# Kernel optimization log

Measured on AMD Instinct MI355X. Metric: run time of the kernel, lower is better.

## Reference

```python
import jax, jax.numpy as jnp
import numpy as np

N_NODES = 100000


def gcn_conv(x, edge_index, W, b, n_nodes):
    # GCNConv: out = D^{-1/2} (A + I) D^{-1/2} X W + b  (add_self_loops=True)
    xw = x @ W  # [N, F_out]
    loop = jnp.arange(n_nodes, dtype=edge_index.dtype)
    row = jnp.concatenate([edge_index[0], loop])  # source
    col = jnp.concatenate([edge_index[1], loop])  # target
    ones = jnp.ones(row.shape[0], dtype=x.dtype)
    deg = jax.ops.segment_sum(ones, col, num_segments=n_nodes)
    dinv = jnp.where(deg > 0, jax.lax.rsqrt(deg), 0.0)
    norm = dinv[row] * dinv[col]  # [E+N]
    msgs = norm[:, None] * xw[row]  # gather + scale
    out = jax.ops.segment_sum(msgs, col, num_segments=n_nodes)  # scatter-add
    return out + b


def setup_inputs() -> dict:
    key = jax.random.key(0)
    k1, k2, k3, k4 = jax.random.split(key, 4)
    x = jax.random.normal(k1, (N_NODES, 512), dtype=jnp.float32)
    edge_index = jax.random.randint(k2, (2, 3200000), 0, N_NODES, dtype=jnp.int64)
    W1 = jax.random.normal(k3, (512, 16), dtype=jnp.float32) * (1.0 / np.sqrt(512))
    b1 = jnp.zeros((16,), dtype=jnp.float32)
    W2 = jax.random.normal(k4, (16, 7), dtype=jnp.float32) * (1.0 / np.sqrt(16))
    b2 = jnp.zeros((7,), dtype=jnp.float32)
    return {"x": x, "edge_index": edge_index, "W1": W1, "b1": b1, "W2": W2, "b2": b2}


def reference(x, edge_index, W1, b1, W2, b2):
    n = x.shape[0]
    h = gcn_conv(x, edge_index, W1, b1, n)
    h = jax.nn.relu(h)
    # F.dropout(training=self.training) is identity in eval mode
    h = gcn_conv(h, edge_index, W2, b2, n)
    return jax.nn.log_softmax(h, axis=1)
```

## Files before the change

kernel.cpp:

```cpp
#include <hip/hip_runtime.h>
#include <math.h>
#include <stdint.h>

#define NBMAX 512
#define BCAP 10240

typedef __attribute__((ext_vector_type(8))) short short8;
typedef __attribute__((ext_vector_type(4))) float f32x4;

__device__ __forceinline__ unsigned int f2bf(float f) {
    unsigned int u = __float_as_uint(f);
    return (u + 0x7FFFu + ((u >> 16) & 1u)) >> 16;
}
__device__ __forceinline__ float bl(unsigned int u) { return __uint_as_float(u << 16); }
__device__ __forceinline__ float bh(unsigned int u) { return __uint_as_float(u & 0xFFFF0000u); }

__global__ void k_zero(int* __restrict__ p, int n) {
    int i = threadIdx.x;
    if (i < n) p[i] = 0;
}

__global__ __launch_bounds__(256) void k_hist_gemm(
    const int* __restrict__ col, int* __restrict__ bucketCnt, int E, int hB, int NB,
    const float* __restrict__ x, const float* __restrict__ W1,
    float* __restrict__ xw, int n) {
    __shared__ union {
        int hist[NBMAX];
        struct { uint4 bhi[1024]; uint4 blo[1024]; } g;
    } sh;
    if (blockIdx.x < hB) {
        for (int t = threadIdx.x; t < NB; t += 256) sh.hist[t] = 0;
        __syncthreads();
        int base = blockIdx.x * 4096;
#pragma unroll
        for (int i = 0; i < 16; ++i) {
            int e = base + threadIdx.x + i * 256;
            if (e < E) atomicAdd(&sh.hist[col[e] >> 8], 1);
        }
        __syncthreads();
        for (int t = threadIdx.x; t < NB; t += 256) {
            int c = sh.hist[t];
            if (c) atomicAdd(&bucketCnt[t], c);
        }
        return;
    }
    for (int s = threadIdx.x; s < 1024; s += 256) {
        int ts = s >> 6, l = s & 63;
        int colc = l & 15, kg = l >> 4;
        int kbase = ts * 32 + kg * 8;
        unsigned int hw[8], lw[8];
#pragma unroll
        for (int j = 0; j < 8; ++j) {
            float wv = W1[(size_t)(kbase + j) * 16 + colc];
            unsigned int u = __float_as_uint(wv);
            unsigned int h = u >> 16;
            unsigned int lo = f2bf(wv - bl(h));
            hw[j] = h; lw[j] = lo;
        }
        uint4 ph, pl;
        ph.x = hw[0] | (hw[1] << 16); ph.y = hw[2] | (hw[3] << 16);
        ph.z = hw[4] | (hw[5] << 16); ph.w = hw[6] | (hw[7] << 16);
        pl.x = lw[0] | (lw[1] << 16); pl.y = lw[2] | (lw[3] << 16);
        pl.z = lw[4] | (lw[5] << 16); pl.w = lw[6] | (lw[7] << 16);
        sh.g.bhi[s] = ph; sh.g.blo[s] = pl;
    }
    __syncthreads();

    int w = threadIdx.x >> 6, lane = threadIdx.x & 63;
    int mtMax = (n + 15) >> 4;
    int mt = (blockIdx.x - hB) * 4 + w;
    if (mt >= mtMax) return;
    int rowbase = mt * 16;
    int r0 = rowbase + (lane & 15);
    if (r0 >= n) r0 = n - 1;
    int kg = lane >> 4;
    const float4* xr = (const float4*)(x + (size_t)r0 * 512);
    f32x4 acc = {0.f, 0.f, 0.f, 0.f};
#pragma unroll 2
    for (int ts = 0; ts < 16; ++ts) {
        float4 u = xr[ts * 8 + kg * 2];
        float4 v = xr[ts * 8 + kg * 2 + 1];
        float e[8] = {u.x, u.y, u.z, u.w, v.x, v.y, v.z, v.w};
        short8 ah, al;
#pragma unroll
        for (int j = 0; j < 8; ++j) {
            unsigned int uu = __float_as_uint(e[j]);
            unsigned int h = uu >> 16;
            unsigned int lo = f2bf(e[j] - bl(h));
            ah[j] = (short)h;
            al[j] = (short)lo;
        }
        uint4 bhw = sh.g.bhi[ts * 64 + lane];
        uint4 blw = sh.g.blo[ts * 64 + lane];
        short8 bhv = *reinterpret_cast<const short8*>(&bhw);
        short8 blv = *reinterpret_cast<const short8*>(&blw);
        acc = __builtin_amdgcn_mfma_f32_16x16x32_bf16(ah, bhv, acc, 0, 0, 0);
        acc = __builtin_amdgcn_mfma_f32_16x16x32_bf16(al, bhv, acc, 0, 0, 0);
        acc = __builtin_amdgcn_mfma_f32_16x16x32_bf16(ah, blv, acc, 0, 0, 0);
    }
#pragma unroll
    for (int r = 0; r < 4; ++r) {
        int orow = rowbase + kg * 4 + r;
        if (orow < n) xw[(size_t)orow * 16 + (lane & 15)] = acc[r];
    }
}

__global__ void k_scanB(const int* __restrict__ bucketCnt, int* __restrict__ baseB,
                        int* __restrict__ cursor, int* __restrict__ offs,
                        int NB, int N, int E) {
    __shared__ int s[512];
    int t = threadIdx.x;
    int c = (t < NB) ? bucketCnt[t] : 0;
    s[t] = c;
    __syncthreads();
    for (int o = 1; o < 512; o <<= 1) {
        int v = (t >= o) ? s[t - o] : 0;
        __syncthreads();
        s[t] += v;
        __syncthreads();
    }
    if (t < NB) { int ex = s[t] - c; baseB[t] = ex; cursor[t] = ex; }
    if (t == NB) baseB[NB] = E;
    if (t == 0) offs[N] = E;
}

__global__ __launch_bounds__(512) void k_bucket(
    const int* __restrict__ row, const int* __restrict__ col,
    int* __restrict__ cursor, unsigned int* __restrict__ sortedG, int E, int NB) {
    __shared__ int histL[NBMAX];
    __shared__ int offsL[NBMAX];
    __shared__ int gbL[NBMAX];
    __shared__ int sbuf[512];
    __shared__ unsigned int stageW[4096];
    __shared__ unsigned short stageB[4096];
    int t = threadIdx.x;
    for (int i = t; i < NB; i += 512) histL[i] = 0;
    __syncthreads();
    int off = blockIdx.x * 4096;
    unsigned int w[8]; int bk[8]; int rk[8];
#pragma unroll
    for (int i = 0; i < 8; ++i) {
        int e = off + t + i * 512;
        if (e < E) {
            int c = col[e], r = row[e];
            w[i]  = ((unsigned int)r << 8) | (unsigned int)(c & 255);
            bk[i] = c >> 8;
            rk[i] = atomicAdd(&histL[bk[i]], 1);
        } else bk[i] = -1;
    }
    __syncthreads();
    int cnt = (t < NB) ? histL[t] : 0;
    sbuf[t] = cnt;
    __syncthreads();
    for (int o = 1; o < 512; o <<= 1) {
        int v = (t >= o) ? sbuf[t - o] : 0;
        __syncthreads();
        sbuf[t] += v;
        __syncthreads();
    }
    if (t < NB) {
        offsL[t] = sbuf[t] - cnt;
        gbL[t]   = cnt ? atomicAdd(&cursor[t], cnt) : 0;
    }
    __syncthreads();
#pragma unroll
    for (int i = 0; i < 8; ++i) {
        if (bk[i] >= 0) {
            int s2 = offsL[bk[i]] + rk[i];
            stageW[s2] = w[i];
            stageB[s2] = (unsigned short)bk[i];
        }
    }
    __syncthreads();
    int total = min(4096, E - off);
    for (int s2 = t; s2 < total; s2 += 512) {
        int b = stageB[s2];
        sortedG[gbL[b] + (s2 - offsL[b])] = stageW[s2];
    }
}

__global__ __launch_bounds__(512) void k_sortscale(
    unsigned int* __restrict__ sortedG, const int* __restrict__ baseB,
    int* __restrict__ offs, float* __restrict__ dinv,
    const float* __restrict__ xw, unsigned int* __restrict__ sxwh, int N) {
    __shared__ unsigned int wv[BCAP];
    __shared__ int hist[256];
    __shared__ int off_[256];
    __shared__ int sc[256];
    __shared__ float ds[256];
    int t = threadIdx.x, b = blockIdx.x;
    if (t < 256) hist[t] = 0;
    __syncthreads();
    int beg = baseB[b], end = baseB[b + 1];
    int cnt = end - beg;
    for (int i = t; i < cnt; i += 512) {
        unsigned int w = sortedG[beg + i];
        wv[i] = w;
        atomicAdd(&hist[w & 255], 1);
    }
    __syncthreads();
    if (t < 256) sc[t] = hist[t];
    __syncthreads();
    for (int o = 1; o < 256; o <<= 1) {
        int v = 0;
        if (t < 256 && t >= o) v = sc[t - o];
        __syncthreads();
        if (t < 256) sc[t] += v;
        __syncthreads();
    }
    if (t < 256) {
        off_[t] = sc[t] - hist[t];
        int node = b * 256 + t;
        float dv = rsqrtf((float)(hist[t] + 1));
        ds[t] = dv;
        if (node < N) { offs[node] = beg + off_[t]; dinv[node] = dv; }
        hist[t] = 0;
    }
    __syncthreads();
    for (int i = t; i < cnt; i += 512) {
        unsigned int w = wv[i];
        int c = w & 255;
        int r2 = atomicAdd(&hist[c], 1);
        sortedG[beg + off_[c] + r2] = w >> 8;
    }
    const float4* xw4 = (const float4*)xw;
    uint2* dsth = (uint2*)sxwh;
#pragma unroll
    for (int k = 0; k < 2; ++k) {
        int idx = t + k * 512;
        int nl  = idx >> 2;
        int node = b * 256 + nl;
        if (node < N) {
            float s = ds[nl];
            float4 v = xw4[(size_t)b * 1024 + idx];
            unsigned int u0 = f2bf(v.x * s), u1 = f2bf(v.y * s);
            unsigned int u2 = f2bf(v.z * s), u3 = f2bf(v.w * s);
            uint2 o; o.x = u0 | (u1 << 16); o.y = u2 | (u3 << 16);
            dsth[(size_t)b * 1024 + idx] = o;
        }
    }
}

__global__ __launch_bounds__(256) void k_gather1f(
    const int* __restrict__ offs, const int* __restrict__ srow,
    const uint4* __restrict__ s4, const float* __restrict__ dinv,
    const float* __restrict__ W2, const float* __restrict__ b1,
    float* __restrict__ sxw2p, int N) {
    __shared__ float sW2[112];
    __shared__ float sb1[16];
    if (threadIdx.x < 112) sW2[threadIdx.x] = W2[threadIdx.x];
    if (threadIdx.x < 16) sb1[threadIdx.x] = b1[threadIdx.x];
    __syncthreads();
    int idx = blockIdx.x * 256 + threadIdx.x;
    int node = idx >> 2, sub = idx & 3;
    int q = sub & 1, seg = sub >> 1;
    if (node >= N) return;
    int beg0 = offs[node], end0 = offs[node + 1];
    int mid = beg0 + ((end0 - beg0) >> 1);
    int beg = seg ? mid : beg0;
    int end = seg ? end0 : mid;

    float a0 = 0.f, a1 = 0.f, a2 = 0.f, a3 = 0.f;
    float a4 = 0.f, a5 = 0.f, a6 = 0.f, a7 = 0.f;
    if (seg == 0) {
        uint4 sv = s4[(size_t)node * 2 + q];
        a0 = bl(sv.x); a1 = bh(sv.x); a2 = bl(sv.y); a3 = bh(sv.y);
        a4 = bl(sv.z); a5 = bh(sv.z); a6 = bl(sv.w); a7 = bh(sv.w);
    }
    int j = beg;
    for (; j + 3 < end; j += 4) {
        int r0 = srow[j], r1 = srow[j + 1], r2 = srow[j + 2], r3 = srow[j + 3];
        uint4 v0 = s4[(size_t)r0 * 2 + q];
        uint4 v1 = s4[(size_t)r1 * 2 + q];
        uint4 v2 = s4[(size_t)r2 * 2 + q];
        uint4 v3 = s4[(size_t)r3 * 2 + q];
        a0 += (bl(v0.x) + bl(v1.x)) + (bl(v2.x) + bl(v3.x));
        a1 += (bh(v0.x) + bh(v1.x)) + (bh(v2.x) + bh(v3.x));
        a2 += (bl(v0.y) + bl(v1.y)) + (bl(v2.y) + bl(v3.y));
        a3 += (bh(v0.y) + bh(v1.y)) + (bh(v2.y) + bh(v3.y));
        a4 += (bl(v0.z) + bl(v1.z)) + (bl(v2.z) + bl(v3.z));
        a5 += (bh(v0.z) + bh(v1.z)) + (bh(v2.z) + bh(v3.z));
        a6 += (bl(v0.w) + bl(v1.w)) + (bl(v2.w) + bl(v3.w));
        a7 += (bh(v0.w) + bh(v1.w)) + (bh(v2.w) + bh(v3.w));
    }
    for (; j < end; ++j) {
        int r = srow[j];
        uint4 v = s4[(size_t)r * 2 + q];
        a0 += bl(v.x); a1 += bh(v.x); a2 += bl(v.y); a3 += bh(v.y);
        a4 += bl(v.z); a5 += bh(v.z); a6 += bl(v.w); a7 += bh(v.w);
    }
    a0 += __shfl_xor(a0, 2, 64); a1 += __shfl_xor(a1, 2, 64);
    a2 += __shfl_xor(a2, 2, 64); a3 += __shfl_xor(a3, 2, 64);
    a4 += __shfl_xor(a4, 2, 64); a5 += __shfl_xor(a5, 2, 64);
    a6 += __shfl_xor(a6, 2, 64); a7 += __shfl_xor(a7, 2, 64);
    float d = dinv[node];
    float h[8];
    h[0] = fmaxf(fmaf(d, a0, sb1[q * 8 + 0]), 0.f);
    h[1] = fmaxf(fmaf(d, a1, sb1[q * 8 + 1]), 0.f);
    h[2] = fmaxf(fmaf(d, a2, sb1[q * 8 + 2]), 0.f);
    h[3] = fmaxf(fmaf(d, a3, sb1[q * 8 + 3]), 0.f);
    h[4] = fmaxf(fmaf(d, a4, sb1[q * 8 + 4]), 0.f);
    h[5] = fmaxf(fmaf(d, a5, sb1[q * 8 + 5]), 0.f);
    h[6] = fmaxf(fmaf(d, a6, sb1[q * 8 + 6]), 0.f);
    h[7] = fmaxf(fmaf(d, a7, sb1[q * 8 + 7]), 0.f);
    float o[7] = {0.f, 0.f, 0.f, 0.f, 0.f, 0.f, 0.f};
    int rbase = q * 8;
#pragma unroll
    for (int i = 0; i < 8; ++i) {
        float hv = h[i];
#pragma unroll
        for (int jj = 0; jj < 7; ++jj) o[jj] = fmaf(hv, sW2[(rbase + i) * 7 + jj], o[jj]);
    }
#pragma unroll
    for (int jj = 0; jj < 7; ++jj) o[jj] += __shfl_xor(o[jj], 1, 64);
    if (seg == 0) {
        float4 wv4;
        if (q == 0) { wv4.x = o[0] * d; wv4.y = o[1] * d; wv4.z = o[2] * d; wv4.w = o[3] * d; }
        else        { wv4.x = o[4] * d; wv4.y = o[5] * d; wv4.z = o[6] * d; wv4.w = 0.f; }
        ((float4*)sxw2p)[(size_t)node * 2 + q] = wv4;
    }
}

__global__ __launch_bounds__(256) void k_gather2f(
    const int* __restrict__ offs, const int* __restrict__ srow,
    const float* __restrict__ sxw2p, const float* __restrict__ dinv,
    const float* __restrict__ b2, float* __restrict__ out, int N) {
    __shared__ float sb2[8];
    if (threadIdx.x < 7) sb2[threadIdx.x] = b2[threadIdx.x];
    if (threadIdx.x == 7) sb2[7] = 0.f;
    __syncthreads();
    int idx = blockIdx.x * 256 + threadIdx.x;
    int node = idx >> 2, sub = idx & 3;
    int q = sub & 1, seg = sub >> 1;
    if (node >= N) return;
    int beg0 = offs[node], end0 = offs[node + 1];
    int mid = beg0 + ((end0 - beg0) >> 1);
    int beg = seg ? mid : beg0;
    int end = seg ? end0 : mid;
    const float4* s4 = (const float4*)sxw2p;
    float4 a = {0.f, 0.f, 0.f, 0.f};
    if (seg == 0) a = s4[(size_t)node * 2 + q];
    int j = beg;
    for (; j + 3 < end; j += 4) {
        int r0 = srow[j], r1 = srow[j + 1], r2 = srow[j + 2], r3 = srow[j + 3];
        float4 v0 = s4[(size_t)r0 * 2 + q];
        float4 v1 = s4[(size_t)r1 * 2 + q];
        float4 v2 = s4[(size_t)r2 * 2 + q];
        float4 v3 = s4[(size_t)r3 * 2 + q];
        a.x += (v0.x + v1.x) + (v2.x + v3.x);
        a.y += (v0.y + v1.y) + (v2.y + v3.y);
        a.z += (v0.z + v1.z) + (v2.z + v3.z);
        a.w += (v0.w + v1.w) + (v2.w + v3.w);
    }
    for (; j < end; ++j) {
        int r = srow[j];
        float4 v = s4[(size_t)r * 2 + q];
        a.x += v.x; a.y += v.y; a.z += v.z; a.w += v.w;
    }
    a.x += __shfl_xor(a.x, 2, 64); a.y += __shfl_xor(a.y, 2, 64);
    a.z += __shfl_xor(a.z, 2, 64); a.w += __shfl_xor(a.w, 2, 64);
    float d = dinv[node];
    float z0 = fmaf(d, a.x, sb2[q * 4 + 0]);
    float z1 = fmaf(d, a.y, sb2[q * 4 + 1]);
    float z2 = fmaf(d, a.z, sb2[q * 4 + 2]);
    float z3 = (q == 0) ? fmaf(d, a.w, sb2[3]) : -INFINITY;
    float m = fmaxf(fmaxf(z0, z1), fmaxf(z2, z3));
    m = fmaxf(m, __shfl_xor(m, 1, 64));
    float s = expf(z0 - m) + expf(z1 - m) + expf(z2 - m) + ((q == 0) ? expf(z3 - m) : 0.f);
    s += __shfl_xor(s, 1, 64);
    float l = m + logf(s);
    if (seg == 0) {
        float* ob = out + (size_t)node * 7;
        if (q == 0) { ob[0] = z0 - l; ob[1] = z1 - l; ob[2] = z2 - l; ob[3] = z3 - l; }
        else        { ob[4] = z0 - l; ob[5] = z1 - l; ob[6] = z2 - l; }
    }
}

extern "C" void kernel_launch(void* const* d_in, const int* in_sizes, int n_in,
                              void* d_out, int out_size, void* d_ws, size_t ws_size,
                              hipStream_t stream) {
    const float* x  = (const float*)d_in[0];
    const int*   ei = (const int*)d_in[1];
    const float* W1 = (const float*)d_in[2];
    const float* b1 = (const float*)d_in[3];
    const float* W2 = (const float*)d_in[4];
    const float* b2 = (const float*)d_in[5];

    int N = in_sizes[0] / 512;
    int E = in_sizes[1] / 2;
    const int* row = ei;
    const int* col = ei + E;

    int NB = (N + 255) >> 8;

    int* bucketCnt = (int*)d_ws;
    int* baseB     = bucketCnt + 512;
    int* cursor    = baseB + 512;
    int* offs      = cursor + 512;
    unsigned int* sortedG = (unsigned int*)(offs + ((N + 4) & ~3));
    float* dinv  = (float*)(sortedG + E);
    float* xw1   = dinv + N;
    unsigned int* sxwh = (unsigned int*)(xw1 + (size_t)16 * N);
    float* sxw2p = xw1;
    float* out   = (float*)d_out;

    int hB = (E + 4095) / 4096;
    int mtMax = (N + 15) / 16;
    int gM = (mtMax + 3) / 4;
    int bB = (E + 4095) / 4096;
    int gP = (4 * N + 255) / 256;

    k_zero     <<<1, 512, 0, stream>>>(bucketCnt, NB);
    k_hist_gemm<<<hB + gM, 256, 0, stream>>>(col, bucketCnt, E, hB, NB, x, W1, xw1, N);
    k_scanB    <<<1, 512, 0, stream>>>(bucketCnt, baseB, cursor, offs, NB, N, E);
    k_bucket   <<<bB, 512, 0, stream>>>(row, col, cursor, sortedG, E, NB);
    k_sortscale<<<NB, 512, 0, stream>>>(sortedG, baseB, offs, dinv, xw1, sxwh, N);
    k_gather1f <<<gP, 256, 0, stream>>>(offs, (const int*)sortedG, (const uint4*)sxwh,
                                        dinv, W2, b1, sxw2p, N);
    k_gather2f <<<gP, 256, 0, stream>>>(offs, (const int*)sortedG, sxw2p, dinv, b2, out, N);
}
```

Measured before the change: 435.6 us.

## Split histogram from GEMM and stage x tiles through swizzled LDS

Separates the fused histogram+GEMM launch into two kernels, so the GEMM blocks no longer share a launch with histogram blocks. The GEMM now loads 64-row tiles of x coalesced (32 threads per row chunk) and converts them once to bf16 hi/lo. It stores them in an XOR-swizzled LDS layout, and the MFMA fragments read from there instead of each lane doing strided float4 loads per row. This aims to improve global-load coalescing on the 200MB x read, at the cost of an extra launch, more LDS use and extra barriers.

```diff
diff --git a/kernel.cpp b/kernel.cpp
--- a/kernel.cpp
+++ b/kernel.cpp
@@ -20,34 +20,37 @@
     if (i < n) p[i] = 0;
 }
 
-__global__ __launch_bounds__(256) void k_hist_gemm(
-    const int* __restrict__ col, int* __restrict__ bucketCnt, int E, int hB, int NB,
+__global__ __launch_bounds__(256) void k_hist(
+    const int* __restrict__ col, int* __restrict__ bucketCnt, int E, int NB) {
+    __shared__ int histL[NBMAX];
+    for (int t = threadIdx.x; t < NB; t += 256) histL[t] = 0;
+    __syncthreads();
+    int base = blockIdx.x * 4096;
+#pragma unroll
+    for (int i = 0; i < 16; ++i) {
+        int e = base + threadIdx.x + i * 256;
+        if (e < E) atomicAdd(&histL[col[e] >> 8], 1);
+    }
+    __syncthreads();
+    for (int t = threadIdx.x; t < NB; t += 256) {
+        int c = histL[t];
+        if (c) atomicAdd(&bucketCnt[t], c);
+    }
+}
+
+__global__ __launch_bounds__(256) void k_gemm(
     const float* __restrict__ x, const float* __restrict__ W1,
     float* __restrict__ xw, int n) {
-    __shared__ union {
-        int hist[NBMAX];
-        struct { uint4 bhi[1024]; uint4 blo[1024]; } g;
-    } sh;
-    if (blockIdx.x < hB) {
-        for (int t = threadIdx.x; t < NB; t += 256) sh.hist[t] = 0;
-        __syncthreads();
-        int base = blockIdx.x * 4096;
-#pragma unroll
-        for (int i = 0; i < 16; ++i) {
-            int e = base + threadIdx.x + i * 256;
-            if (e < E) atomicAdd(&sh.hist[col[e] >> 8], 1);
-        }
-        __syncthreads();
-        for (int t = threadIdx.x; t < NB; t += 256) {
-            int c = sh.hist[t];
-            if (c) atomicAdd(&bucketCnt[t], c);
-        }
-        return;
-    }
-    for (int s = threadIdx.x; s < 1024; s += 256) {
+    __shared__ uint4 sbhi[1024];
+    __shared__ uint4 sblo[1024];
+    __shared__ unsigned short sxhi[8192];
+    __shared__ unsigned short sxlo[8192];
+    int t = threadIdx.x;
+
+    for (int s = t; s < 1024; s += 256) {
         int ts = s >> 6, l = s & 63;
-        int colc = l & 15, kg = l >> 4;
-        int kbase = ts * 32 + kg * 8;
+        int colc = l & 15, kg2 = l >> 4;
+        int kbase = ts * 32 + kg2 * 8;
         unsigned int hw[8], lw[8];
 #pragma unroll
         for (int j = 0; j < 8; ++j) {
@@ -62,45 +65,64 @@
         ph.z = hw[4] | (hw[5] << 16); ph.w = hw[6] | (hw[7] << 16);
         pl.x = lw[0] | (lw[1] << 16); pl.y = lw[2] | (lw[3] << 16);
         pl.z = lw[4] | (lw[5] << 16); pl.w = lw[6] | (lw[7] << 16);
-        sh.g.bhi[s] = ph; sh.g.blo[s] = pl;
-    }
-    __syncthreads();
-
-    int w = threadIdx.x >> 6, lane = threadIdx.x & 63;
-    int mtMax = (n + 15) >> 4;
-    int mt = (blockIdx.x - hB) * 4 + w;
-    if (mt >= mtMax) return;
-    int rowbase = mt * 16;
-    int r0 = rowbase + (lane & 15);
-    if (r0 >= n) r0 = n - 1;
+        sbhi[s] = ph; sblo[s] = pl;
+    }
+
+    int base = blockIdx.x * 64;
+    int w = t >> 6, lane = t & 63;
     int kg = lane >> 4;
-    const float4* xr = (const float4*)(x + (size_t)r0 * 512);
+    int arow = (w << 4) + (lane & 15);
     f32x4 acc = {0.f, 0.f, 0.f, 0.f};
-#pragma unroll 2
-    for (int ts = 0; ts < 16; ++ts) {
-        float4 u = xr[ts * 8 + kg * 2];
-        float4 v = xr[ts * 8 + kg * 2 + 1];
-        float e[8] = {u.x, u.y, u.z, u.w, v.x, v.y, v.z, v.w};
-        short8 ah, al;
-#pragma unroll
-        for (int j = 0; j < 8; ++j) {
-            unsigned int uu = __float_as_uint(e[j]);
-            unsigned int h = uu >> 16;
-            unsigned int lo = f2bf(e[j] - bl(h));
-            ah[j] = (short)h;
-            al[j] = (short)lo;
-        }
-        uint4 bhw = sh.g.bhi[ts * 64 + lane];
-        uint4 blw = sh.g.blo[ts * 64 + lane];
-        short8 bhv = *reinterpret_cast<const short8*>(&bhw);
-        short8 blv = *reinterpret_cast<const short8*>(&blw);
-        acc = __builtin_amdgcn_mfma_f32_16x16x32_bf16(ah, bhv, acc, 0, 0, 0);
-        acc = __builtin_amdgcn_mfma_f32_16x16x32_bf16(al, bhv, acc, 0, 0, 0);
-        acc = __builtin_amdgcn_mfma_f32_16x16x32_bf16(ah, blv, acc, 0, 0, 0);
+
+    for (int c = 0; c < 4; ++c) {
+        float4 xv[8];
+#pragma unroll
+        for (int i = 0; i < 8; ++i) {
+            int row = i * 8 + (t >> 5);
+            int gr = base + row; if (gr >= n) gr = n - 1;
+            xv[i] = ((const float4*)(x + (size_t)gr * 512 + c * 128))[t & 31];
+        }
+        __syncthreads();
+#pragma unroll
+        for (int i = 0; i < 8; ++i) {
+            int row = i * 8 + (t >> 5);
+            int off = row * 256 + (t & 31) * 8;
+            int swz = off ^ ((row & 7) << 4);
+            float e0 = xv[i].x, e1 = xv[i].y, e2 = xv[i].z, e3 = xv[i].w;
+            unsigned int u0 = __float_as_uint(e0) >> 16;
+            unsigned int u1 = __float_as_uint(e1) >> 16;
+            unsigned int u2 = __float_as_uint(e2) >> 16;
+            unsigned int u3 = __float_as_uint(e3) >> 16;
+            ushort4 hv, lv;
+            hv.x = (unsigned short)u0; hv.y = (unsigned short)u1;
+            hv.z = (unsigned short)u2; hv.w = (unsigned short)u3;
+            lv.x = (unsigned short)f2bf(e0 - bl(u0));
+            lv.y = (unsigned short)f2bf(e1 - bl(u1));
+            lv.z = (unsigned short)f2bf(e2 - bl(u2));
+            lv.w = (unsigned short)f2bf(e3 - bl(u3));
+            *(ushort4*)((char*)sxhi + swz) = hv;
+            *(ushort4*)((char*)sxlo + swz) = lv;
+        }
+        __syncthreads();
+#pragma unroll
+        for (int ts = 0; ts < 4; ++ts) {
+            int off = arow * 256 + ts * 64 + kg * 16;
+            int swz = off ^ ((arow & 7) << 4);
+            short8 ah = *(const short8*)((const char*)sxhi + swz);
+            short8 al = *(const short8*)((const char*)sxlo + swz);
+            int tsg = c * 4 + ts;
+            uint4 bhw = sbhi[tsg * 64 + lane];
+            uint4 blw = sblo[tsg * 64 + lane];
+            short8 bh_ = *reinterpret_cast<const short8*>(&bhw);
+            short8 bl_ = *reinterpret_cast<const short8*>(&blw);
+            acc = __builtin_amdgcn_mfma_f32_16x16x32_bf16(ah, bh_, acc, 0, 0, 0);
+            acc = __builtin_amdgcn_mfma_f32_16x16x32_bf16(al, bh_, acc, 0, 0, 0);
+            acc = __builtin_amdgcn_mfma_f32_16x16x32_bf16(ah, bl_, acc, 0, 0, 0);
+        }
     }
 #pragma unroll
     for (int r = 0; r < 4; ++r) {
-        int orow = rowbase + kg * 4 + r;
+        int orow = base + (w << 4) + kg * 4 + r;
         if (orow < n) xw[(size_t)orow * 16 + (lane & 15)] = acc[r];
     }
 }
@@ -405,13 +427,13 @@
     float* out   = (float*)d_out;
 
     int hB = (E + 4095) / 4096;
-    int mtMax = (N + 15) / 16;
-    int gM = (mtMax + 3) / 4;
+    int gG = (N + 63) / 64;
     int bB = (E + 4095) / 4096;
     int gP = (4 * N + 255) / 256;
 
     k_zero     <<<1, 512, 0, stream>>>(bucketCnt, NB);
-    k_hist_gemm<<<hB + gM, 256, 0, stream>>>(col, bucketCnt, E, hB, NB, x, W1, xw1, N);
+    k_hist     <<<hB, 256, 0, stream>>>(col, bucketCnt, E, NB);
+    k_gemm     <<<gG, 256, 0, stream>>>(x, W1, xw1, N);
     k_scanB    <<<1, 512, 0, stream>>>(bucketCnt, baseB, cursor, offs, NB, N, E);
     k_bucket   <<<bB, 512, 0, stream>>>(row, col, cursor, sortedG, E, NB);
     k_sortscale<<<NB, 512, 0, stream>>>(sortedG, baseB, offs, dinv, xw1, sxwh, N);
```

Result: no change. 443.2 us (+1.7%).

## Replace two-level bucket sort with per-node degree count and atomic scatter CSR build

Applied to the files above, without the earlier changes.

Replaces the bucketed radix-style CSR construction (block-local histograms, bucket staging, per-bucket shared-memory sort) with a direct approach. Per-node degrees are counted with global atomics, bucket sums are reduced, and offsets are scanned. Each edge is then scattered into place through an atomic cursor per node. This cuts the kernel count and the shared-memory staging work, but adds heavy global atomic traffic (3.2M atomics on 100K counters twice) and makes neighbour order within a node nondeterministic, which can affect both the scatter write locality and the gather read pattern.

```diff
diff --git a/kernel.cpp b/kernel.cpp
--- a/kernel.cpp
+++ b/kernel.cpp
@@ -2,9 +2,6 @@
 #include <math.h>
 #include <stdint.h>
 
-#define NBMAX 512
-#define BCAP 10240
-
 typedef __attribute__((ext_vector_type(8))) short short8;
 typedef __attribute__((ext_vector_type(4))) float f32x4;
 
@@ -16,38 +13,28 @@
 __device__ __forceinline__ float bh(unsigned int u) { return __uint_as_float(u & 0xFFFF0000u); }
 
 __global__ void k_zero(int* __restrict__ p, int n) {
-    int i = threadIdx.x;
+    int i = blockIdx.x * 512 + threadIdx.x;
     if (i < n) p[i] = 0;
 }
 
-__global__ __launch_bounds__(256) void k_hist_gemm(
-    const int* __restrict__ col, int* __restrict__ bucketCnt, int E, int hB, int NB,
+__global__ __launch_bounds__(256) void k_deg_gemm(
+    const int* __restrict__ col, int* __restrict__ deg, int E, int dB,
     const float* __restrict__ x, const float* __restrict__ W1,
     float* __restrict__ xw, int n) {
-    __shared__ union {
-        int hist[NBMAX];
-        struct { uint4 bhi[1024]; uint4 blo[1024]; } g;
-    } sh;
-    if (blockIdx.x < hB) {
-        for (int t = threadIdx.x; t < NB; t += 256) sh.hist[t] = 0;
-        __syncthreads();
+    __shared__ struct { uint4 bhi[1024]; uint4 blo[1024]; } sh;
+    if (blockIdx.x < dB) {
         int base = blockIdx.x * 4096;
 #pragma unroll
         for (int i = 0; i < 16; ++i) {
             int e = base + threadIdx.x + i * 256;
-            if (e < E) atomicAdd(&sh.hist[col[e] >> 8], 1);
-        }
-        __syncthreads();
-        for (int t = threadIdx.x; t < NB; t += 256) {
-            int c = sh.hist[t];
-            if (c) atomicAdd(&bucketCnt[t], c);
+            if (e < E) atomicAdd(&deg[col[e]], 1);
         }
         return;
     }
     for (int s = threadIdx.x; s < 1024; s += 256) {
         int ts = s >> 6, l = s & 63;
-        int colc = l & 15, kg = l >> 4;
-        int kbase = ts * 32 + kg * 8;
+        int colc = l & 15, kg2 = l >> 4;
+        int kbase = ts * 32 + kg2 * 8;
         unsigned int hw[8], lw[8];
 #pragma unroll
         for (int j = 0; j < 8; ++j) {
@@ -62,13 +49,13 @@
         ph.z = hw[4] | (hw[5] << 16); ph.w = hw[6] | (hw[7] << 16);
         pl.x = lw[0] | (lw[1] << 16); pl.y = lw[2] | (lw[3] << 16);
         pl.z = lw[4] | (lw[5] << 16); pl.w = lw[6] | (lw[7] << 16);
-        sh.g.bhi[s] = ph; sh.g.blo[s] = pl;
+        sh.bhi[s] = ph; sh.blo[s] = pl;
     }
     __syncthreads();
 
     int w = threadIdx.x >> 6, lane = threadIdx.x & 63;
     int mtMax = (n + 15) >> 4;
-    int mt = (blockIdx.x - hB) * 4 + w;
+    int mt = (blockIdx.x - dB) * 4 + w;
     if (mt >= mtMax) return;
     int rowbase = mt * 16;
     int r0 = rowbase + (lane & 15);
@@ -90,8 +77,8 @@
             ah[j] = (short)h;
             al[j] = (short)lo;
         }
-        uint4 bhw = sh.g.bhi[ts * 64 + lane];
-        uint4 blw = sh.g.blo[ts * 64 + lane];
+        uint4 bhw = sh.bhi[ts * 64 + lane];
+        uint4 blw = sh.blo[ts * 64 + lane];
         short8 bhv = *reinterpret_cast<const short8*>(&bhw);
         short8 blv = *reinterpret_cast<const short8*>(&blw);
         acc = __builtin_amdgcn_mfma_f32_16x16x32_bf16(ah, bhv, acc, 0, 0, 0);
@@ -105,9 +92,22 @@
     }
 }
 
+__global__ __launch_bounds__(256) void k_bsum(
+    const int* __restrict__ deg, int* __restrict__ bucketCnt, int N) {
+    __shared__ int s[256];
+    int t = threadIdx.x;
+    int node = blockIdx.x * 256 + t;
+    s[t] = (node < N) ? deg[node] : 0;
+    __syncthreads();
+    for (int o = 128; o > 0; o >>= 1) {
+        if (t < o) s[t] += s[t + o];
+        __syncthreads();
+    }
+    if (t == 0) bucketCnt[blockIdx.x] = s[0];
+}
+
 __global__ void k_scanB(const int* __restrict__ bucketCnt, int* __restrict__ baseB,
-                        int* __restrict__ cursor, int* __restrict__ offs,
-                        int NB, int N, int E) {
+                        int* __restrict__ offs, int NB, int N, int E) {
     __shared__ int s[512];
     int t = threadIdx.x;
     int c = (t < NB) ? bucketCnt[t] : 0;
@@ -119,87 +119,24 @@
         s[t] += v;
         __syncthreads();
     }
-    if (t < NB) { int ex = s[t] - c; baseB[t] = ex; cursor[t] = ex; }
+    if (t < NB) baseB[t] = s[t] - c;
     if (t == NB) baseB[NB] = E;
     if (t == 0) offs[N] = E;
 }
 
-__global__ __launch_bounds__(512) void k_bucket(
-    const int* __restrict__ row, const int* __restrict__ col,
-    int* __restrict__ cursor, unsigned int* __restrict__ sortedG, int E, int NB) {
-    __shared__ int histL[NBMAX];
-    __shared__ int offsL[NBMAX];
-    __shared__ int gbL[NBMAX];
-    __shared__ int sbuf[512];
-    __shared__ unsigned int stageW[4096];
-    __shared__ unsigned short stageB[4096];
-    int t = threadIdx.x;
-    for (int i = t; i < NB; i += 512) histL[i] = 0;
-    __syncthreads();
-    int off = blockIdx.x * 4096;
-    unsigned int w[8]; int bk[8]; int rk[8];
-#pragma unroll
-    for (int i = 0; i < 8; ++i) {
-        int e = off + t + i * 512;
-        if (e < E) {
-            int c = col[e], r = row[e];
-            w[i]  = ((unsigned int)r << 8) | (unsigned int)(c & 255);
-            bk[i] = c >> 8;
-            rk[i] = atomicAdd(&histL[bk[i]], 1);
-        } else bk[i] = -1;
-    }
-    __syncthreads();
-    int cnt = (t < NB) ? histL[t] : 0;
-    sbuf[t] = cnt;
-    __syncthreads();
-    for (int o = 1; o < 512; o <<= 1) {
-        int v = (t >= o) ? sbuf[t - o] : 0;
-        __syncthreads();
-        sbuf[t] += v;
-        __syncthreads();
-    }
-    if (t < NB) {
-        offsL[t] = sbuf[t] - cnt;
-        gbL[t]   = cnt ? atomicAdd(&cursor[t], cnt) : 0;
-    }
-    __syncthreads();
-#pragma unroll
-    for (int i = 0; i < 8; ++i) {
-        if (bk[i] >= 0) {
-            int s2 = offsL[bk[i]] + rk[i];
-            stageW[s2] = w[i];
-            stageB[s2] = (unsigned short)bk[i];
-        }
-    }
-    __syncthreads();
-    int total = min(4096, E - off);
-    for (int s2 = t; s2 < total; s2 += 512) {
-        int b = stageB[s2];
-        sortedG[gbL[b] + (s2 - offsL[b])] = stageW[s2];
-    }
-}
-
-__global__ __launch_bounds__(512) void k_sortscale(
-    unsigned int* __restrict__ sortedG, const int* __restrict__ baseB,
-    int* __restrict__ offs, float* __restrict__ dinv,
+__global__ __launch_bounds__(512) void k_offs(
+    const int* __restrict__ deg, const int* __restrict__ baseB,
+    int* __restrict__ offs, int* __restrict__ cursor, float* __restrict__ dinv,
     const float* __restrict__ xw, unsigned int* __restrict__ sxwh, int N) {
-    __shared__ unsigned int wv[BCAP];
-    __shared__ int hist[256];
-    __shared__ int off_[256];
     __shared__ int sc[256];
     __shared__ float ds[256];
     int t = threadIdx.x, b = blockIdx.x;
-    if (t < 256) hist[t] = 0;
-    __syncthreads();
-    int beg = baseB[b], end = baseB[b + 1];
-    int cnt = end - beg;
-    for (int i = t; i < cnt; i += 512) {
-        unsigned int w = sortedG[beg + i];
-        wv[i] = w;
-        atomicAdd(&hist[w & 255], 1);
-    }
-    __syncthreads();
-    if (t < 256) sc[t] = hist[t];
+    int d = 0;
+    if (t < 256) {
+        int node = b * 256 + t;
+        d = (node < N) ? deg[node] : 0;
+        sc[t] = d;
+    }
     __syncthreads();
     for (int o = 1; o < 256; o <<= 1) {
         int v = 0;
@@ -209,20 +146,13 @@
         __syncthreads();
     }
     if (t < 256) {
-        off_[t] = sc[t] - hist[t];
         int node = b * 256 + t;
-        float dv = rsqrtf((float)(hist[t] + 1));
+        int pos = baseB[b] + sc[t] - d;
+        float dv = rsqrtf((float)(d + 1));
         ds[t] = dv;
-        if (node < N) { offs[node] = beg + off_[t]; dinv[node] = dv; }
-        hist[t] = 0;
-    }
-    __syncthreads();
-    for (int i = t; i < cnt; i += 512) {
-        unsigned int w = wv[i];
-        int c = w & 255;
-        int r2 = atomicAdd(&hist[c], 1);
-        sortedG[beg + off_[c] + r2] = w >> 8;
-    }
+        if (node < N) { offs[node] = pos; cursor[node] = pos; dinv[node] = dv; }
+    }
+    __syncthreads();
     const float4* xw4 = (const float4*)xw;
     uint2* dsth = (uint2*)sxwh;
 #pragma unroll
@@ -237,6 +167,21 @@
             unsigned int u2 = f2bf(v.z * s), u3 = f2bf(v.w * s);
             uint2 o; o.x = u0 | (u1 << 16); o.y = u2 | (u3 << 16);
             dsth[(size_t)b * 1024 + idx] = o;
+        }
+    }
+}
+
+__global__ __launch_bounds__(512) void k_scatter(
+    const int* __restrict__ row, const int* __restrict__ col,
+    int* __restrict__ cursor, int* __restrict__ sortedG, int E) {
+    int off = blockIdx.x * 4096;
+#pragma unroll
+    for (int i = 0; i < 8; ++i) {
+        int e = off + threadIdx.x + i * 512;
+        if (e < E) {
+            int c = col[e];
+            int pos = atomicAdd(&cursor[c], 1);
+            sortedG[pos] = row[e];
         }
     }
 }
@@ -395,27 +340,29 @@
 
     int* bucketCnt = (int*)d_ws;
     int* baseB     = bucketCnt + 512;
-    int* cursor    = baseB + 512;
-    int* offs      = cursor + 512;
-    unsigned int* sortedG = (unsigned int*)(offs + ((N + 4) & ~3));
+    int* deg       = baseB + 512;
+    int* cursor    = deg + ((N + 4) & ~3);
+    int* offs      = cursor + ((N + 4) & ~3);
+    int* sortedG   = offs + ((N + 4) & ~3);
     float* dinv  = (float*)(sortedG + E);
     float* xw1   = dinv + N;
     unsigned int* sxwh = (unsigned int*)(xw1 + (size_t)16 * N);
     float* sxw2p = xw1;
     float* out   = (float*)d_out;
 
-    int hB = (E + 4095) / 4096;
+    int dB = (E + 4095) / 4096;
     int mtMax = (N + 15) / 16;
     int gM = (mtMax + 3) / 4;
     int bB = (E + 4095) / 4096;
     int gP = (4 * N + 255) / 256;
 
-    k_zero     <<<1, 512, 0, stream>>>(bucketCnt, NB);
-    k_hist_gemm<<<hB + gM, 256, 0, stream>>>(col, bucketCnt, E, hB, NB, x, W1, xw1, N);
-    k_scanB    <<<1, 512, 0, stream>>>(bucketCnt, baseB, cursor, offs, NB, N, E);
-    k_bucket   <<<bB, 512, 0, stream>>>(row, col, cursor, sortedG, E, NB);
-    k_sortscale<<<NB, 512, 0, stream>>>(sortedG, baseB, offs, dinv, xw1, sxwh, N);
-    k_gather1f <<<gP, 256, 0, stream>>>(offs, (const int*)sortedG, (const uint4*)sxwh,
-                                        dinv, W2, b1, sxw2p, N);
-    k_gather2f <<<gP, 256, 0, stream>>>(offs, (const int*)sortedG, sxw2p, dinv, b2, out, N);
-}
+    k_zero    <<<(N + 511) / 512, 512, 0, stream>>>(deg, N);
+    k_deg_gemm<<<dB + gM, 256, 0, stream>>>(col, deg, E, dB, x, W1, xw1, N);
+    k_bsum    <<<NB, 256, 0, stream>>>(deg, bucketCnt, N);
+    k_scanB   <<<1, 512, 0, stream>>>(bucketCnt, baseB, offs, NB, N, E);
+    k_offs    <<<NB, 512, 0, stream>>>(deg, baseB, offs, cursor, dinv, xw1, sxwh, N);
+    k_scatter <<<bB, 512, 0, stream>>>(row, col, cursor, sortedG, E);
+    k_gather1f<<<gP, 256, 0, stream>>>(offs, sortedG, (const uint4*)sxwh,
+                                       dinv, W2, b1, sxw2p, N);
+    k_gather2f<<<gP, 256, 0, stream>>>(offs, sortedG, sxw2p, dinv, b2, out, N);
+}
```

Result: slower. 750.4 us (+72.3%).
